# Optimization experiments

Measured on AMD Instinct MI355X. Metric: run time of the kernel, lower is better.

## Reference

```python
import jax, jax.numpy as jnp
import numpy as np

B, N, H = 32, 1024, 128
EPS = 1e-5


def setup_inputs() -> dict:
    key = jax.random.key(0)
    ks = jax.random.split(key, 9)
    node_embeddings = jax.random.normal(ks[0], (B, N, H), dtype=jnp.float32)
    edge_relations = jax.random.normal(ks[1], (B, N, N, 3), dtype=jnp.float32)
    adjacency = jax.random.randint(ks[2], (N, N), 0, 2, dtype=jnp.int32)
    s_msg = 1.0 / np.sqrt(H + 3)
    s_upd = 1.0 / np.sqrt(2 * H)
    W_msg = jax.random.uniform(ks[3], (H, H + 3), jnp.float32, -s_msg, s_msg)
    b_msg = jax.random.uniform(ks[4], (H,), jnp.float32, -s_msg, s_msg)
    W_upd = jax.random.uniform(ks[5], (H, 2 * H), jnp.float32, -s_upd, s_upd)
    b_upd = jax.random.uniform(ks[6], (H,), jnp.float32, -s_upd, s_upd)
    gamma = jnp.ones((H,), jnp.float32)
    beta = jnp.zeros((H,), jnp.float32)
    return {"node_embeddings": node_embeddings, "edge_relations": edge_relations,
            "adjacency": adjacency, "W_msg": W_msg, "b_msg": b_msg,
            "W_upd": W_upd, "b_upd": b_upd, "gamma": gamma, "beta": beta}


def reference(node_embeddings, edge_relations, adjacency, W_msg, b_msg, W_upd, b_upd, gamma, beta):
    # node_embeddings: [B,N,H]; edge_relations: [B,N,N,3]; adjacency: [N,N]
    b_, n_, h_ = node_embeddings.shape
    mask = (adjacency > 0).astype(node_embeddings.dtype)  # mask[j,i]=1 if i is neighbor of j
    # Split msg_nn weight: Linear(cat(h_i, e_ij)) = h_i @ W_h^T + e_ij @ W_e^T + b
    W_h = W_msg[:, :h_]   # [H,H]
    W_e = W_msg[:, h_:]   # [H,3]
    h_part = jnp.einsum('bih,oh->bio', node_embeddings, W_h)       # [B,N,H]
    msg_h = jnp.einsum('ji,bio->bjo', mask, h_part)                # aggregate sender linear part
    e_agg = jnp.einsum('bijc,ji->bjc', edge_relations, mask)       # aggregate edge feats first (memory-bound)
    msg_e = jnp.einsum('bjc,oc->bjo', e_agg, W_e)
    deg = mask.sum(axis=1)                                         # [N] in-degree of j
    messages = msg_h + msg_e + deg[None, :, None] * b_msg          # bias added once per edge
    # Dropout(0.2) is identity in inference; BatchNorm uses batch stats (training-mode math).
    upd_in = jnp.concatenate([node_embeddings, messages], axis=-1)  # [B,N,2H]
    updated = jax.nn.relu(jnp.einsum('bjk,ok->bjo', upd_in, W_upd) + b_upd)
    flat = updated.reshape(-1, h_)
    mean = flat.mean(axis=0)
    var = flat.var(axis=0)  # biased, as BatchNorm1d
    normed = (flat - mean) * jax.lax.rsqrt(var + EPS) * gamma + beta
    return normed.reshape(b_, n_, h_) + node_embeddings
```

## Files before the change

### kernel.cpp

```cpp
#include <hip/hip_runtime.h>

typedef _Float16 f16;
typedef f16 f16x4 __attribute__((ext_vector_type(4)));
typedef f16 f16x8 __attribute__((ext_vector_type(8)));
typedef float f32x4 __attribute__((ext_vector_type(4)));

#define BB 32
#define NN 1024
#define HH 128
#define ROWS (BB*NN)
#define EPS 1e-5f

__device__ __forceinline__ f16 f2h(float x) { return (f16)x; }

typedef __attribute__((address_space(1))) const void gv_t;
typedef __attribute__((address_space(3))) void lv_t;
__device__ __forceinline__ void gl_lds16(const void* g, void* l) {
  __builtin_amdgcn_global_load_lds((gv_t*)g, (lv_t*)l, 16, 0, 0);
}

__global__ __launch_bounds__(256) void prep0_k(
    const float* __restrict__ W_msg, const float* __restrict__ W_upd,
    const float* __restrict__ node, const int* __restrict__ adj,
    f16* __restrict__ Wh, f16* __restrict__ Wupd, float* __restrict__ We,
    f16* __restrict__ nodeh, f16* __restrict__ maskf, f16* __restrict__ maskT)
{
  const int blk = blockIdx.x, t = threadIdx.x;
  if (blk < 64) {
    const long base = (long)blk*16384 + t;
    #pragma unroll
    for (int p = 0; p < 64; p++) {
      const long idx = base + (long)p*256;
      const float4 v = ((const float4*)node)[idx];
      f16x4 hv; hv[0] = f2h(v.x); hv[1] = f2h(v.y); hv[2] = f2h(v.z); hv[3] = f2h(v.w);
      *(f16x4*)&nodeh[idx << 2] = hv;
    }
  } else if (blk < 128) {
    __shared__ f16 ldsT[128][136];
    const int tt = blk - 64, tj = tt >> 3, ti = tt & 7;
    #pragma unroll
    for (int p = 0; p < 16; p++) {
      const int q = p*256 + t;
      const int row = q >> 5, c4 = (q & 31) << 2;
      const int4 m = *(const int4*)&adj[(long)(tj*128 + row)*NN + ti*128 + c4];
      f16x4 hv;
      hv[0] = (m.x > 0) ? (f16)1.0f : (f16)0.0f;
      hv[1] = (m.y > 0) ? (f16)1.0f : (f16)0.0f;
      hv[2] = (m.z > 0) ? (f16)1.0f : (f16)0.0f;
      hv[3] = (m.w > 0) ? (f16)1.0f : (f16)0.0f;
      *(f16x4*)&maskf[(long)(tj*128 + row)*NN + ti*128 + c4] = hv;
      ldsT[c4 + 0][row] = hv[0];
      ldsT[c4 + 1][row] = hv[1];
      ldsT[c4 + 2][row] = hv[2];
      ldsT[c4 + 3][row] = hv[3];
    }
    __syncthreads();
    #pragma unroll
    for (int p = 0; p < 8; p++) {
      const int q = p*256 + t;
      const int rT = q >> 4, c8 = (q & 15) << 3;
      *(uint4*)&maskT[(long)(ti*128 + rT)*NN + tj*128 + c8] =
          *(const uint4*)&ldsT[rT][c8];
    }
  } else if (blk == 128) {
    for (int idx = t; idx < HH*HH; idx += 256) {
      const int o = idx >> 7, h = idx & 127;
      Wh[idx] = f2h(W_msg[o*131 + h]);
    }
  } else if (blk == 129) {
    for (int idx = t; idx < HH*256; idx += 256)
      Wupd[idx] = f2h(W_upd[idx]);
  } else {
    for (int idx = t; idx < HH*3; idx += 256)
      We[idx] = W_msg[(idx/3)*131 + 128 + (idx % 3)];
  }
}

__global__ __launch_bounds__(256) void phaseB_k(
    const f16* __restrict__ nodeh, const float* __restrict__ E,
    const f16* __restrict__ maskT, const f16* __restrict__ Wh,
    const float* __restrict__ b_msg,
    f16* __restrict__ h_part_T, float* __restrict__ e_agg)
{
  __shared__ __align__(16) char smem[24576];
  const int tid = threadIdx.x;

  if (blockIdx.x >= 256) {
    float* Ebuf = (float*)smem;
    const int e  = blockIdx.x - 256;
    const int bb = e >> 5;
    const int r5 = e & 31;
    const int jt = r5 & 3;
    const int ih = r5 >> 2;
    const int j  = (jt << 8) + tid;
    const int i0 = ih << 7;
    const int lane = tid & 63, wv = tid >> 6;
    const float* Eblk = E + (long)bb*3145728 + (long)i0*3072 + (long)(jt << 8)*3;
    float a0 = 0.f, a1 = 0.f, a2 = 0.f;
    for (int ch = 0; ch < 16; ch++) {
      const float* Ech = Eblk + (long)ch*8*3072;
      __syncthreads();
      #pragma unroll
      for (int k = 0; k < 6; k++) {
        const int m = wv*6 + k;
        const int r = m/3;
        const int cb = (m % 3) << 8;
        gl_lds16(Ech + (long)r*3072 + cb + lane*4, Ebuf + m*256);
      }
      float mreg[8];
      #pragma unroll
      for (int v = 0; v < 8; v++)
        mreg[v] = (float)maskT[(long)(i0 + ch*8 + v)*NN + j];
      __syncthreads();
      #pragma unroll
      for (int v = 0; v < 8; v++) {
        const float e0 = Ebuf[v*768 + tid*3];
        const float e1 = Ebuf[v*768 + tid*3 + 1];
        const float e2 = Ebuf[v*768 + tid*3 + 2];
        a0 = fmaf(mreg[v], e0, a0);
        a1 = fmaf(mreg[v], e1, a1);
        a2 = fmaf(mreg[v], e2, a2);
      }
    }
    const long eb = ((long)bb*NN + j)*3;
    atomicAdd(&e_agg[eb],     a0);
    atomicAdd(&e_agg[eb + 1], a1);
    atomicAdd(&e_agg[eb + 2], a2);
    return;
  }

  f16* As = (f16*)smem;
  f16* Bs = (f16*)(smem + 8192);
  const int g  = blockIdx.x;
  const int nt = g & 7, bb = g >> 3;
  const int nbase = nt << 7;
  const int lane = tid & 63, wave = tid >> 6;
  const int wm = (wave & 1) << 6, wn = (wave >> 1) << 6;

  f32x4 acc[2][4], acc2[2][4];
  #pragma unroll
  for (int i = 0; i < 2; i++)
    #pragma unroll
    for (int j = 0; j < 4; j++)
      #pragma unroll
      for (int r = 0; r < 4; r++) { acc[i][j][r] = 0.f; acc2[i][j][r] = 0.f; }

  for (int k0 = 0; k0 < HH; k0 += 32) {
    #pragma unroll
    for (int p = 0; p < 2; p++) {
      const int q = (p << 8) + tid;
      const int row = q >> 2, kp = (q & 3) << 3;
      gl_lds16(&Wh[(long)row*HH + k0 + kp], &As[q << 3]);
      gl_lds16(&nodeh[(long)((bb << 10) + nbase + row)*HH + k0 + kp], &Bs[q << 3]);
    }
    __syncthreads();
    f16x8 af[4], bf[4];
    #pragma unroll
    for (int i = 0; i < 4; i++) {
      af[i] = *(const f16x8*)&As[((wm + (i << 4) + (lane & 15)) << 5) + ((lane >> 4) << 3)];
      bf[i] = *(const f16x8*)&Bs[((wn + (i << 4) + (lane & 15)) << 5) + ((lane >> 4) << 3)];
    }
    #pragma unroll
    for (int i = 0; i < 2; i++)
      #pragma unroll
      for (int j = 0; j < 4; j++) {
        acc[i][j]  = __builtin_amdgcn_mfma_f32_16x16x32_f16(af[i],     bf[j], acc[i][j],  0, 0, 0);
        acc2[i][j] = __builtin_amdgcn_mfma_f32_16x16x32_f16(af[i + 2], bf[j], acc2[i][j], 0, 0, 0);
      }
    __syncthreads();
  }

  f16* out = h_part_T + (long)bb * (HH*NN);
  const int rb = (lane >> 4) << 2, cb = lane & 15;
  #pragma unroll
  for (int i = 0; i < 4; i++)
    #pragma unroll
    for (int r = 0; r < 4; r++) {
      const int gm = wm + (i << 4) + rb + r;
      const float bm = b_msg[gm];
      #pragma unroll
      for (int j = 0; j < 4; j++) {
        const int gn = nbase + wn + (j << 4) + cb;
        const float v = ((i < 2) ? acc[i][j][r] : acc2[i - 2][j][r]) + bm;
        out[(long)gm*NN + gn] = f2h(v);
      }
    }
}

__global__ __launch_bounds__(256) void gemm1_k(
    const f16* __restrict__ maskf, const f16* __restrict__ hp,
    const float* __restrict__ e_agg, const float* __restrict__ We,
    f16* __restrict__ msgs)
{
  const int mt = blockIdx.x, bb = blockIdx.z;
  const int jb = mt << 7;
  __shared__ f16 As[128*32];
  __shared__ f16 Bs[128*32];
  const int tid = threadIdx.x, lane = tid & 63, wave = tid >> 6;
  const int wm = (wave & 1) << 6, wn = (wave >> 1) << 6;

  f32x4 acc[4][4];
  #pragma unroll
  for (int i = 0; i < 4; i++)
    #pragma unroll
    for (int j = 0; j < 4; j++)
      #pragma unroll
      for (int r = 0; r < 4; r++) acc[i][j][r] = 0.f;

  for (int k0 = 0; k0 < NN; k0 += 32) {
    #pragma unroll
    for (int p = 0; p < 2; p++) {
      const int q = (p << 8) + tid;
      const int row = q >> 2, kp = (q & 3) << 3;
      gl_lds16(&maskf[(long)(jb + row)*NN + k0 + kp], &As[q << 3]);
      gl_lds16(&hp[(long)bb*(HH*NN) + (long)row*NN + k0 + kp], &Bs[q << 3]);
    }
    __syncthreads();
    f16x8 af[4], bf[4];
    #pragma unroll
    for (int i = 0; i < 4; i++) {
      af[i] = *(const f16x8*)&As[((wm + (i << 4) + (lane & 15)) << 5) + ((lane >> 4) << 3)];
      bf[i] = *(const f16x8*)&Bs[((wn + (i << 4) + (lane & 15)) << 5) + ((lane >> 4) << 3)];
    }
    #pragma unroll
    for (int i = 0; i < 4; i++)
      #pragma unroll
      for (int j = 0; j < 4; j++)
        acc[i][j] = __builtin_amdgcn_mfma_f32_16x16x32_f16(af[i], bf[j], acc[i][j], 0, 0, 0);
    __syncthreads();
  }

  const int rb = (lane >> 4) << 2, cb = lane & 15;
  #pragma unroll
  for (int i = 0; i < 4; i++)
    #pragma unroll
    for (int r = 0; r < 4; r++) {
      const int gm = jb + wm + (i << 4) + rb + r;
      const long eb = ((long)bb*NN + gm)*3;
      const float e0 = e_agg[eb], e1 = e_agg[eb+1], e2 = e_agg[eb+2];
      #pragma unroll
      for (int j = 0; j < 4; j++) {
        const int gn = wn + (j << 4) + cb;
        const float v = acc[i][j][r]
                      + e0*We[gn*3] + e1*We[gn*3+1] + e2*We[gn*3+2];
        msgs[((long)bb*NN + gm)*HH + gn] = f2h(v);
      }
    }
}

__global__ __launch_bounds__(256) void gemm2_k(
    const f16* __restrict__ nodeh, const f16* __restrict__ msgs,
    const f16* __restrict__ Wupd, const float* __restrict__ b_upd,
    f16* __restrict__ upd, float* __restrict__ sums)
{
  const int mt = blockIdx.x;
  const int rowb = mt << 7;
  __shared__ f16 As[128*32];
  __shared__ f16 Bs[128*32];
  __shared__ float colS[128], colQ[128];
  const int tid = threadIdx.x, lane = tid & 63, wave = tid >> 6;
  const int wm = (wave & 1) << 6, wn = (wave >> 1) << 6;
  if (tid < 128) { colS[tid] = 0.f; colQ[tid] = 0.f; }

  f32x4 acc[4][4];
  #pragma unroll
  for (int i = 0; i < 4; i++)
    #pragma unroll
    for (int j = 0; j < 4; j++)
      #pragma unroll
      for (int r = 0; r < 4; r++) acc[i][j][r] = 0.f;

  for (int k0 = 0; k0 < 256; k0 += 32) {
    #pragma unroll
    for (int p = 0; p < 2; p++) {
      const int q = (p << 8) + tid;
      const int row = q >> 2, kp = (q & 3) << 3;
      const f16* src = (k0 < HH)
        ? &nodeh[(long)(rowb + row)*HH + k0 + kp]
        : &msgs[(long)(rowb + row)*HH + (k0 - HH) + kp];
      gl_lds16(src, &As[q << 3]);
      gl_lds16(&Wupd[(long)row*256 + k0 + kp], &Bs[q << 3]);
    }
    __syncthreads();
    f16x8 af[4], bf[4];
    #pragma unroll
    for (int i = 0; i < 4; i++) {
      af[i] = *(const f16x8*)&As[((wm + (i << 4) + (lane & 15)) << 5) + ((lane >> 4) << 3)];
      bf[i] = *(const f16x8*)&Bs[((wn + (i << 4) + (lane & 15)) << 5) + ((lane >> 4) << 3)];
    }
    #pragma unroll
    for (int i = 0; i < 4; i++)
      #pragma unroll
      for (int j = 0; j < 4; j++)
        acc[i][j] = __builtin_amdgcn_mfma_f32_16x16x32_f16(af[i], bf[j], acc[i][j], 0, 0, 0);
    __syncthreads();
  }

  const int rb = (lane >> 4) << 2, cb = lane & 15;
  float bup[4], s[4] = {0,0,0,0}, qq[4] = {0,0,0,0};
  #pragma unroll
  for (int j = 0; j < 4; j++) bup[j] = b_upd[wn + (j << 4) + cb];
  #pragma unroll
  for (int i = 0; i < 4; i++)
    #pragma unroll
    for (int r = 0; r < 4; r++) {
      const int gm = rowb + wm + (i << 4) + rb + r;
      #pragma unroll
      for (int j = 0; j < 4; j++) {
        const int gn = wn + (j << 4) + cb;
        const float v = fmaxf(acc[i][j][r] + bup[j], 0.f);
        upd[(long)gm*HH + gn] = f2h(v);
        s[j] += v; qq[j] += v*v;
      }
    }
  #pragma unroll
  for (int j = 0; j < 4; j++) {
    const int gn = wn + (j << 4) + cb;
    atomicAdd(&colS[gn], s[j]);
    atomicAdd(&colQ[gn], qq[j]);
  }
  __syncthreads();
  if (tid < 128) {
    atomicAdd(&sums[tid],       colS[tid]);
    atomicAdd(&sums[128 + tid], colQ[tid]);
  }
}

__global__ __launch_bounds__(256) void final_k(const f16* __restrict__ upd,
    const float* __restrict__ node, const float* __restrict__ sums,
    const float* __restrict__ gamma, const float* __restrict__ beta,
    float* __restrict__ out)
{
  const long idx = (long)blockIdx.x*256 + threadIdx.x;
  const f16x4 u  = *(const f16x4*)&upd[idx << 2];
  const float4 nd = ((const float4*)node)[idx];
  const int ob = (idx & 31) << 2;
  const float inv = 1.0f/32768.0f;
  float4 res;
  #pragma unroll
  for (int c = 0; c < 4; c++) {
    const float m  = sums[ob + c]*inv;
    const float va = sums[128 + ob + c]*inv - m*m;
    const float sc = rsqrtf(va + EPS)*gamma[ob + c];
    ((float*)&res)[c] = ((float)u[c] - m)*sc + beta[ob + c]
                      + ((const float*)&nd)[c];
  }
  ((float4*)out)[idx] = res;
}

extern "C" void kernel_launch(void* const* d_in, const int* in_sizes, int n_in,
                              void* d_out, int out_size, void* d_ws, size_t ws_size,
                              hipStream_t stream) {
  const float* node  = (const float*)d_in[0];
  const float* E     = (const float*)d_in[1];
  const int*   adj   = (const int*)  d_in[2];
  const float* W_msg = (const float*)d_in[3];
  const float* b_msg = (const float*)d_in[4];
  const float* W_upd = (const float*)d_in[5];
  const float* b_upd = (const float*)d_in[6];
  const float* gamma = (const float*)d_in[7];
  const float* beta  = (const float*)d_in[8];
  float* out = (float*)d_out;

  char* p = (char*)d_ws;
  auto alloc = [&](size_t n) { void* r = (void*)p; p += (n + 255) & ~(size_t)255; return r; };
  f16*   h_part_T = (f16*)  alloc((size_t)BB*HH*NN*2);
  f16*   msgs     = (f16*)  alloc((size_t)ROWS*HH*2);
  f16*   upd      = (f16*)  alloc((size_t)ROWS*HH*2);
  f16*   nodeh    = (f16*)  alloc((size_t)ROWS*HH*2);
  f16*   maskf    = (f16*)  alloc((size_t)NN*NN*2);
  f16*   maskT    = (f16*)  alloc((size_t)NN*NN*2);
  float* e_agg    = (float*)alloc((size_t)BB*NN*3*4);
  f16*   Wh       = (f16*)  alloc((size_t)HH*HH*2);
  f16*   Wupd     = (f16*)  alloc((size_t)HH*256*2);
  float* We       = (float*)alloc((size_t)HH*3*4);
  float* sums     = (float*)alloc((size_t)256*4);

  hipMemsetAsync(e_agg, 0, (size_t)BB*NN*3*4, stream);
  hipMemsetAsync(sums,  0, (size_t)256*4, stream);

  prep0_k<<<131, 256, 0, stream>>>(W_msg, W_upd, node, adj,
                                   Wh, Wupd, We, nodeh, maskf, maskT);

  phaseB_k<<<1280, 256, 0, stream>>>(nodeh, E, maskT, Wh, b_msg, h_part_T, e_agg);

  gemm1_k<<<dim3(8, 1, BB), 256, 0, stream>>>(maskf, h_part_T, e_agg, We, msgs);

  gemm2_k<<<256, 256, 0, stream>>>(nodeh, msgs, Wupd, b_upd, upd, sums);

  final_k<<<4096, 256, 0, stream>>>(upd, node, sums, gamma, beta, out);
}
```

Baseline: 643.2 us.

## Fuse message GEMM with update GEMM, fold memsets into prep, split edge aggregation finer

The message GEMM now keeps its 128x128 f16 output tile in swizzled shared memory and feeds it straight into the update GEMM and BatchNorm statistics. This removes the msgs global round trip and one kernel launch. The zeroing of e_agg and sums moves into extra prep blocks in place of hipMemsetAsync calls. The edge-aggregation part of phaseB now splits each batch over twice as many blocks with half the rows each, to expose more parallelism at the cost of more atomics. The fused kernel uses about 32KB more LDS per block, which may lower occupancy.

```diff
diff --git a/kernel.cpp b/kernel.cpp
--- a/kernel.cpp
+++ b/kernel.cpp
@@ -23,7 +23,8 @@
     const float* __restrict__ W_msg, const float* __restrict__ W_upd,
     const float* __restrict__ node, const int* __restrict__ adj,
     f16* __restrict__ Wh, f16* __restrict__ Wupd, float* __restrict__ We,
-    f16* __restrict__ nodeh, f16* __restrict__ maskf, f16* __restrict__ maskT)
+    f16* __restrict__ nodeh, f16* __restrict__ maskf, f16* __restrict__ maskT,
+    float* __restrict__ e_agg, float* __restrict__ sums)
 {
   const int blk = blockIdx.x, t = threadIdx.x;
   if (blk < 64) {
@@ -70,9 +71,14 @@
   } else if (blk == 129) {
     for (int idx = t; idx < HH*256; idx += 256)
       Wupd[idx] = f2h(W_upd[idx]);
-  } else {
+  } else if (blk == 130) {
     for (int idx = t; idx < HH*3; idx += 256)
       We[idx] = W_msg[(idx/3)*131 + 128 + (idx % 3)];
+    if (t < 256) sums[t] = 0.f;
+  } else {
+    const int base = (blk - 131) * 24576 + t;
+    #pragma unroll
+    for (int r = 0; r < 96; r++) e_agg[base + r*256] = 0.f;
   }
 }
 
@@ -88,16 +94,16 @@
   if (blockIdx.x >= 256) {
     float* Ebuf = (float*)smem;
     const int e  = blockIdx.x - 256;
-    const int bb = e >> 5;
-    const int r5 = e & 31;
-    const int jt = r5 & 3;
-    const int ih = r5 >> 2;
+    const int bb = e >> 6;
+    const int r6 = e & 63;
+    const int jt = r6 & 3;
+    const int ih = r6 >> 2;
     const int j  = (jt << 8) + tid;
-    const int i0 = ih << 7;
+    const int i0 = ih << 6;
     const int lane = tid & 63, wv = tid >> 6;
     const float* Eblk = E + (long)bb*3145728 + (long)i0*3072 + (long)(jt << 8)*3;
     float a0 = 0.f, a1 = 0.f, a2 = 0.f;
-    for (int ch = 0; ch < 16; ch++) {
+    for (int ch = 0; ch < 8; ch++) {
       const float* Ech = Eblk + (long)ch*8*3072;
       __syncthreads();
       #pragma unroll
@@ -187,17 +193,24 @@
     }
 }
 
-__global__ __launch_bounds__(256) void gemm1_k(
+__global__ __launch_bounds__(256) void gemm12_k(
     const f16* __restrict__ maskf, const f16* __restrict__ hp,
     const float* __restrict__ e_agg, const float* __restrict__ We,
-    f16* __restrict__ msgs)
+    const f16* __restrict__ nodeh, const f16* __restrict__ Wupd,
+    const float* __restrict__ b_upd,
+    f16* __restrict__ upd, float* __restrict__ sums)
 {
   const int mt = blockIdx.x, bb = blockIdx.z;
   const int jb = mt << 7;
+  const long rowb = (long)bb*NN + jb;
   __shared__ f16 As[128*32];
   __shared__ f16 Bs[128*32];
+  __shared__ __align__(16) char msgs_lds[128*128*2];
+  __shared__ float colS[128], colQ[128];
   const int tid = threadIdx.x, lane = tid & 63, wave = tid >> 6;
   const int wm = (wave & 1) << 6, wn = (wave >> 1) << 6;
+  if (tid < 128) { colS[tid] = 0.f; colQ[tid] = 0.f; }
+  const int rb = (lane >> 4) << 2, cb = lane & 15;
 
   f32x4 acc[4][4];
   #pragma unroll
@@ -230,73 +243,64 @@
     __syncthreads();
   }
 
-  const int rb = (lane >> 4) << 2, cb = lane & 15;
   #pragma unroll
   for (int i = 0; i < 4; i++)
     #pragma unroll
     for (int r = 0; r < 4; r++) {
-      const int gm = jb + wm + (i << 4) + rb + r;
-      const long eb = ((long)bb*NN + gm)*3;
+      const int lrow = wm + (i << 4) + rb + r;
+      const long eb = (rowb + lrow)*3;
       const float e0 = e_agg[eb], e1 = e_agg[eb+1], e2 = e_agg[eb+2];
       #pragma unroll
       for (int j = 0; j < 4; j++) {
-        const int gn = wn + (j << 4) + cb;
+        const int col = wn + (j << 4) + cb;
         const float v = acc[i][j][r]
-                      + e0*We[gn*3] + e1*We[gn*3+1] + e2*We[gn*3+2];
-        msgs[((long)bb*NN + gm)*HH + gn] = f2h(v);
-      }
-    }
-}
-
-__global__ __launch_bounds__(256) void gemm2_k(
-    const f16* __restrict__ nodeh, const f16* __restrict__ msgs,
-    const f16* __restrict__ Wupd, const float* __restrict__ b_upd,
-    f16* __restrict__ upd, float* __restrict__ sums)
-{
-  const int mt = blockIdx.x;
-  const int rowb = mt << 7;
-  __shared__ f16 As[128*32];
-  __shared__ f16 Bs[128*32];
-  __shared__ float colS[128], colQ[128];
-  const int tid = threadIdx.x, lane = tid & 63, wave = tid >> 6;
-  const int wm = (wave & 1) << 6, wn = (wave >> 1) << 6;
-  if (tid < 128) { colS[tid] = 0.f; colQ[tid] = 0.f; }
-
-  f32x4 acc[4][4];
+                      + e0*We[col*3] + e1*We[col*3+1] + e2*We[col*3+2];
+        const int byte = ((lrow << 8) + (col << 1)) ^ ((lrow & 7) << 4);
+        *(f16*)(msgs_lds + byte) = f2h(v);
+      }
+    }
+  __syncthreads();
+
+  f32x4 acc2[4][4];
   #pragma unroll
   for (int i = 0; i < 4; i++)
     #pragma unroll
     for (int j = 0; j < 4; j++)
       #pragma unroll
-      for (int r = 0; r < 4; r++) acc[i][j][r] = 0.f;
+      for (int r = 0; r < 4; r++) acc2[i][j][r] = 0.f;
 
   for (int k0 = 0; k0 < 256; k0 += 32) {
+    const bool fromA = (k0 < HH);
     #pragma unroll
     for (int p = 0; p < 2; p++) {
       const int q = (p << 8) + tid;
       const int row = q >> 2, kp = (q & 3) << 3;
-      const f16* src = (k0 < HH)
-        ? &nodeh[(long)(rowb + row)*HH + k0 + kp]
-        : &msgs[(long)(rowb + row)*HH + (k0 - HH) + kp];
-      gl_lds16(src, &As[q << 3]);
+      if (fromA)
+        gl_lds16(&nodeh[(rowb + row)*HH + k0 + kp], &As[q << 3]);
       gl_lds16(&Wupd[(long)row*256 + k0 + kp], &Bs[q << 3]);
     }
     __syncthreads();
     f16x8 af[4], bf[4];
     #pragma unroll
     for (int i = 0; i < 4; i++) {
-      af[i] = *(const f16x8*)&As[((wm + (i << 4) + (lane & 15)) << 5) + ((lane >> 4) << 3)];
+      if (fromA) {
+        af[i] = *(const f16x8*)&As[((wm + (i << 4) + (lane & 15)) << 5) + ((lane >> 4) << 3)];
+      } else {
+        const int lrow = wm + (i << 4) + (lane & 15);
+        const int byte = ((lrow << 8) + (((k0 - HH) + ((lane >> 4) << 3)) << 1))
+                         ^ ((lrow & 7) << 4);
+        af[i] = *(const f16x8*)(msgs_lds + byte);
+      }
       bf[i] = *(const f16x8*)&Bs[((wn + (i << 4) + (lane & 15)) << 5) + ((lane >> 4) << 3)];
     }
     #pragma unroll
     for (int i = 0; i < 4; i++)
       #pragma unroll
       for (int j = 0; j < 4; j++)
-        acc[i][j] = __builtin_amdgcn_mfma_f32_16x16x32_f16(af[i], bf[j], acc[i][j], 0, 0, 0);
-    __syncthreads();
-  }
-
-  const int rb = (lane >> 4) << 2, cb = lane & 15;
+        acc2[i][j] = __builtin_amdgcn_mfma_f32_16x16x32_f16(af[i], bf[j], acc2[i][j], 0, 0, 0);
+    __syncthreads();
+  }
+
   float bup[4], s[4] = {0,0,0,0}, qq[4] = {0,0,0,0};
   #pragma unroll
   for (int j = 0; j < 4; j++) bup[j] = b_upd[wn + (j << 4) + cb];
@@ -304,12 +308,12 @@
   for (int i = 0; i < 4; i++)
     #pragma unroll
     for (int r = 0; r < 4; r++) {
-      const int gm = rowb + wm + (i << 4) + rb + r;
+      const long gm = rowb + wm + (i << 4) + rb + r;
       #pragma unroll
       for (int j = 0; j < 4; j++) {
         const int gn = wn + (j << 4) + cb;
-        const float v = fmaxf(acc[i][j][r] + bup[j], 0.f);
-        upd[(long)gm*HH + gn] = f2h(v);
+        const float v = fmaxf(acc2[i][j][r] + bup[j], 0.f);
+        upd[gm*HH + gn] = f2h(v);
         s[j] += v; qq[j] += v*v;
       }
     }
@@ -365,7 +369,6 @@
   char* p = (char*)d_ws;
   auto alloc = [&](size_t n) { void* r = (void*)p; p += (n + 255) & ~(size_t)255; return r; };
   f16*   h_part_T = (f16*)  alloc((size_t)BB*HH*NN*2);
-  f16*   msgs     = (f16*)  alloc((size_t)ROWS*HH*2);
   f16*   upd      = (f16*)  alloc((size_t)ROWS*HH*2);
   f16*   nodeh    = (f16*)  alloc((size_t)ROWS*HH*2);
   f16*   maskf    = (f16*)  alloc((size_t)NN*NN*2);
@@ -376,17 +379,14 @@
   float* We       = (float*)alloc((size_t)HH*3*4);
   float* sums     = (float*)alloc((size_t)256*4);
 
-  hipMemsetAsync(e_agg, 0, (size_t)BB*NN*3*4, stream);
-  hipMemsetAsync(sums,  0, (size_t)256*4, stream);
-
-  prep0_k<<<131, 256, 0, stream>>>(W_msg, W_upd, node, adj,
-                                   Wh, Wupd, We, nodeh, maskf, maskT);
-
-  phaseB_k<<<1280, 256, 0, stream>>>(nodeh, E, maskT, Wh, b_msg, h_part_T, e_agg);
-
-  gemm1_k<<<dim3(8, 1, BB), 256, 0, stream>>>(maskf, h_part_T, e_agg, We, msgs);
-
-  gemm2_k<<<256, 256, 0, stream>>>(nodeh, msgs, Wupd, b_upd, upd, sums);
+  prep0_k<<<135, 256, 0, stream>>>(W_msg, W_upd, node, adj,
+                                   Wh, Wupd, We, nodeh, maskf, maskT,
+                                   e_agg, sums);
+
+  phaseB_k<<<2304, 256, 0, stream>>>(nodeh, E, maskT, Wh, b_msg, h_part_T, e_agg);
+
+  gemm12_k<<<dim3(8, 1, BB), 256, 0, stream>>>(maskf, h_part_T, e_agg, We,
+                                               nodeh, Wupd, b_upd, upd, sums);
 
   final_k<<<4096, 256, 0, stream>>>(upd, node, sums, gamma, beta, out);
 }
```

Result: no change. 630.7 us (-1.9%).
